# Kernel tuning notes

Hardware: AMD Instinct MI355X
Metric: run time of the kernel (lower is better)

Reference implementation:

```python
import jax, jax.numpy as jnp
import numpy as np

B, N, DIM = 2, 2048, 1024
HEADS, DIM_HEAD = 16, 64
SCALE = DIM_HEAD ** -0.5
MASK_VALUE = -jnp.finfo(jnp.float32).max


def setup_inputs() -> dict:
    key = jax.random.key(0)
    ks = jax.random.split(key, 7)
    inner = HEADS * DIM_HEAD
    x = jax.random.normal(ks[0], (B, N, DIM), dtype=jnp.float32)
    mask = jax.random.randint(ks[1], (B, 1, N, N), 0, 2, dtype=jnp.int32)
    Wq = jax.random.normal(ks[2], (DIM, inner), dtype=jnp.float32) * (DIM ** -0.5)
    Wk = jax.random.normal(ks[3], (DIM, inner), dtype=jnp.float32) * (DIM ** -0.5)
    Wv = jax.random.normal(ks[4], (DIM, inner), dtype=jnp.float32) * (DIM ** -0.5)
    Wo = jax.random.normal(ks[5], (inner, DIM), dtype=jnp.float32) * (inner ** -0.5)
    bo = jnp.zeros((DIM,), dtype=jnp.float32)
    return {"x": x, "mask": mask, "Wq": Wq, "Wk": Wk, "Wv": Wv, "Wo": Wo, "bo": bo}


def reference(x, mask, Wq, Wk, Wv, Wo, bo):
    b, n, _ = x.shape
    # projections -> [b, h, n, d]
    def split_heads(t):
        return t.reshape(b, n, HEADS, DIM_HEAD).transpose(0, 2, 1, 3)
    q = split_heads(x @ Wq)
    k = split_heads(x @ Wk)
    v = split_heads(x @ Wv)
    # full attention scores [b, h, i, j]
    dots = jnp.einsum('bhid,bhjd->bhij', q, k) * SCALE
    # faithful to source: bin_mask = (mask == 0); fill where ~bin_mask
    bin_mask = (mask == 0)
    dots = jnp.where(bin_mask, dots, MASK_VALUE)
    attn = jax.nn.softmax(dots, axis=-1)  # dropout p=0.0 -> identity
    out = jnp.einsum('bhij,bhjd->bhid', attn, v)
    out = out.transpose(0, 2, 1, 3).reshape(b, n, HEADS * DIM_HEAD)
    return out @ Wo + bo
```

## Files before the change

### kernel.cpp

```cpp
#include <hip/hip_runtime.h>
#include <cstdint>
#include <cstddef>

typedef float    f32x4  __attribute__((ext_vector_type(4)));
typedef __bf16   bf16x8 __attribute__((ext_vector_type(8)));
typedef unsigned u32x4  __attribute__((ext_vector_type(4)));
typedef unsigned u32x2  __attribute__((ext_vector_type(2)));
typedef unsigned short u16;
typedef unsigned int   u32;

#define SCL2E 0.18033688011112042f

static __device__ __forceinline__ u16 f2bf(float f) {
    u32 u = __builtin_bit_cast(u32, f);
    u32 r = (u + 0x7FFFu + ((u >> 16) & 1u)) >> 16;
    return (u16)r;
}

static __device__ __forceinline__ u32 cvtpk_bf16(float lo, float hi) {
    u32 r;
    asm("v_cvt_pk_bf16_f32 %0, %1, %2" : "=v"(r) : "v"(lo), "v"(hi));
    return r;
}

static __device__ __forceinline__ float fexp2(float x) {
    float r;
    asm("v_exp_f32 %0, %1" : "=v"(r) : "v"(x));
    return r;
}

static __device__ __forceinline__ void gll16(const u16* g, void* l) {
    __builtin_amdgcn_global_load_lds((const __attribute__((address_space(1))) void*)g,
                                     (__attribute__((address_space(3))) void*)l, 16, 0, 0);
}


__global__ __launch_bounds__(256) void prep_k(
    const float* __restrict__ x, u16* __restrict__ xb,
    const float* __restrict__ W0, const float* __restrict__ W1,
    const float* __restrict__ W2, const float* __restrict__ W3,
    u16* __restrict__ T0, u16* __restrict__ T1,
    u16* __restrict__ T2, u16* __restrict__ T3,
    const int* __restrict__ mask, u32* __restrict__ mp)
{
    __shared__ float T[64][65];
    const int bid = blockIdx.x;
    if (bid < 2048) {
        const long i = ((long)bid * 256 + threadIdx.x) * 8;
        f32x4 a = *(const f32x4*)(x + i);
        f32x4 c = *(const f32x4*)(x + i + 4);
        u32x4 o;
        o[0] = (u32)f2bf(a[0]) | ((u32)f2bf(a[1]) << 16);
        o[1] = (u32)f2bf(a[2]) | ((u32)f2bf(a[3]) << 16);
        o[2] = (u32)f2bf(c[0]) | ((u32)f2bf(c[1]) << 16);
        o[3] = (u32)f2bf(c[2]) | ((u32)f2bf(c[3]) << 16);
        *(u32x4*)(xb + i) = o;
    } else if (bid < 3072) {
        const int idx = bid - 2048;
        const int z = idx >> 8, rem = idx & 255;
        const int n0 = (rem & 15) * 64, k0 = (rem >> 4) * 64;
        const float* W = (z == 0) ? W0 : (z == 1) ? W1 : (z == 2) ? W2 : W3;
        u16* Wt = (z == 0) ? T0 : (z == 1) ? T1 : (z == 2) ? T2 : T3;
        const float scl = (z == 0) ? SCL2E : 1.0f;
        const int c = threadIdx.x & 63, r0 = (threadIdx.x >> 6) * 16;
#pragma unroll
        for (int i = 0; i < 16; ++i)
            T[r0 + i][c] = W[(long)(k0 + r0 + i) * 1024 + n0 + c];
        __syncthreads();
#pragma unroll
        for (int i = 0; i < 16; ++i)
            Wt[(long)(n0 + r0 + i) * 1024 + k0 + c] = f2bf(T[c][r0 + i] * scl);
    } else {
        const long wi = (long)(bid - 3072) * 256 + threadIdx.x;
        const int* src = mask + wi * 32;
        u32 word = 0;
#pragma unroll
        for (int c = 0; c < 8; ++c) {
            const int4 v = *(const int4*)(src + c * 4);
            word |= (u32)(v.x != 0) << (c * 4);
            word |= (u32)(v.y != 0) << (c * 4 + 1);
            word |= (u32)(v.z != 0) << (c * 4 + 2);
            word |= (u32)(v.w != 0) << (c * 4 + 3);
        }
        mp[wi] = word;
    }
}

__global__ __launch_bounds__(256) void vt_k(const u16* __restrict__ v, u16* __restrict__ vt) {
    __shared__ u16 T[64][66];
    const int nt = blockIdx.x, h = blockIdx.y, b = blockIdx.z;
    const int c = threadIdx.x & 63, r0 = (threadIdx.x >> 6) * 16;
    const u16* src = v + ((long)b * 2048 + nt * 64) * 1024 + h * 64;
    u16* dst = vt + ((long)(b * 16 + h) * 64) * 2048 + nt * 64;
#pragma unroll
    for (int i = 0; i < 16; ++i)
        T[r0 + i][c] = src[(long)(r0 + i) * 1024 + c];
    __syncthreads();
#pragma unroll
    for (int i = 0; i < 16; ++i)
        dst[(long)(r0 + i) * 2048 + c] = T[c][r0 + i];
}


__global__ __launch_bounds__(256, 3) void gemm_qkv(
    const u16* __restrict__ A, const u16* __restrict__ Bt, u16* __restrict__ C0)
{
    constexpr int K = 1024;
    __shared__ u16 As[2][128 * 32];
    __shared__ u16 Bs[2][128 * 32];
    const int tid = threadIdx.x;
    const int wave = tid >> 6, lane = tid & 63;
    const int wr = wave >> 1, wc = wave & 1;
    const int g = lane >> 4, lr = lane & 15;
    const long mBase = (long)blockIdx.y * 128;
    const long nBase = (long)blockIdx.x * 128;

    f32x4 acc[4][4];
#pragma unroll
    for (int i = 0; i < 4; ++i)
#pragma unroll
        for (int j = 0; j < 4; ++j) acc[i][j] = f32x4{0.f, 0.f, 0.f, 0.f};

    const int o0 = tid * 16, o1 = (256 + tid) * 16;
    const int r0 = o0 >> 6, cb0 = o0 & 63;
    const int r1 = o1 >> 6, cb1 = o1 & 63;

    gll16(A  + (mBase + r0) * K + (cb0 >> 1), (char*)&As[0][0] + o0);
    gll16(A  + (mBase + r1) * K + (cb1 >> 1), (char*)&As[0][0] + o1);
    gll16(Bt + (nBase + r0) * K + (cb0 >> 1), (char*)&Bs[0][0] + o0);
    gll16(Bt + (nBase + r1) * K + (cb1 >> 1), (char*)&Bs[0][0] + o1);
    __syncthreads();

#pragma unroll 2
    for (int kt = 0; kt < 32; ++kt) {
        const int buf = kt & 1;
        if (kt + 1 < 32) {
            const long ko = (long)(kt + 1) * 32;
            gll16(A  + (mBase + r0) * K + ko + (cb0 >> 1), (char*)&As[buf ^ 1][0] + o0);
            gll16(A  + (mBase + r1) * K + ko + (cb1 >> 1), (char*)&As[buf ^ 1][0] + o1);
            gll16(Bt + (nBase + r0) * K + ko + (cb0 >> 1), (char*)&Bs[buf ^ 1][0] + o0);
            gll16(Bt + (nBase + r1) * K + ko + (cb1 >> 1), (char*)&Bs[buf ^ 1][0] + o1);
        }
        bf16x8 af[4], bfv[4];
#pragma unroll
        for (int mi = 0; mi < 4; ++mi)
            af[mi] = *(const bf16x8*)((const char*)&As[buf][0] + (wr * 64 + mi * 16 + lr) * 64 + g * 16);
#pragma unroll
        for (int ni = 0; ni < 4; ++ni)
            bfv[ni] = *(const bf16x8*)((const char*)&Bs[buf][0] + (wc * 64 + ni * 16 + lr) * 64 + g * 16);
#pragma unroll
        for (int mi = 0; mi < 4; ++mi)
#pragma unroll
            for (int ni = 0; ni < 4; ++ni)
                acc[mi][ni] = __builtin_amdgcn_mfma_f32_16x16x32_bf16(af[mi], bfv[ni], acc[mi][ni], 0, 0, 0);
        __syncthreads();
    }

    const int wsel = (int)(nBase >> 10);
    u16* Cw = C0 + (long)wsel * (4096l * 1024);
    const long ncl = nBase & 1023;
#pragma unroll
    for (int mi = 0; mi < 4; ++mi)
#pragma unroll
        for (int r = 0; r < 4; ++r) {
            const long row = mBase + wr * 64 + mi * 16 + g * 4 + r;
#pragma unroll
            for (int ni = 0; ni < 4; ++ni) {
                const long col = ncl + wc * 64 + ni * 16 + lr;
                Cw[row * 1024 + col] = f2bf(acc[mi][ni][r]);
            }
        }
}


__global__ __launch_bounds__(256, 2) void gemm_out(
    const u16* __restrict__ A, const u16* __restrict__ Bt,
    float* __restrict__ Cf, const float* __restrict__ bias)
{
    constexpr int K = 1024, N = 1024;
    __shared__ u16 As[2][64 * 32];
    __shared__ u16 Bs[2][128 * 32];
    const int tid = threadIdx.x;
    const int wave = tid >> 6, lane = tid & 63;
    const int wr = wave >> 1, wc = wave & 1;
    const int g = lane >> 4, lr = lane & 15;
    const long mBase = (long)blockIdx.y * 64;
    const long nBase = (long)blockIdx.x * 128;

    f32x4 acc[2][4];
#pragma unroll
    for (int i = 0; i < 2; ++i)
#pragma unroll
        for (int j = 0; j < 4; ++j) acc[i][j] = f32x4{0.f, 0.f, 0.f, 0.f};

    const int oA = tid * 16;
    const int rA = oA >> 6, cbA = oA & 63;
    const int o0 = tid * 16, o1 = (256 + tid) * 16;
    const int r0 = o0 >> 6, cb0 = o0 & 63;
    const int r1 = o1 >> 6, cb1 = o1 & 63;

    gll16(A  + (mBase + rA) * K + (cbA >> 1), (char*)&As[0][0] + oA);
    gll16(Bt + (nBase + r0) * K + (cb0 >> 1), (char*)&Bs[0][0] + o0);
    gll16(Bt + (nBase + r1) * K + (cb1 >> 1), (char*)&Bs[0][0] + o1);
    __syncthreads();

#pragma unroll 2
    for (int kt = 0; kt < 32; ++kt) {
        const int buf = kt & 1;
        if (kt + 1 < 32) {
            const long ko = (long)(kt + 1) * 32;
            gll16(A  + (mBase + rA) * K + ko + (cbA >> 1), (char*)&As[buf ^ 1][0] + oA);
            gll16(Bt + (nBase + r0) * K + ko + (cb0 >> 1), (char*)&Bs[buf ^ 1][0] + o0);
            gll16(Bt + (nBase + r1) * K + ko + (cb1 >> 1), (char*)&Bs[buf ^ 1][0] + o1);
        }
        bf16x8 af[2], bfv[4];
#pragma unroll
        for (int mi = 0; mi < 2; ++mi)
            af[mi] = *(const bf16x8*)((const char*)&As[buf][0] + (wr * 32 + mi * 16 + lr) * 64 + g * 16);
#pragma unroll
        for (int ni = 0; ni < 4; ++ni)
            bfv[ni] = *(const bf16x8*)((const char*)&Bs[buf][0] + (wc * 64 + ni * 16 + lr) * 64 + g * 16);
#pragma unroll
        for (int mi = 0; mi < 2; ++mi)
#pragma unroll
            for (int ni = 0; ni < 4; ++ni)
                acc[mi][ni] = __builtin_amdgcn_mfma_f32_16x16x32_bf16(af[mi], bfv[ni], acc[mi][ni], 0, 0, 0);
        __syncthreads();
    }

#pragma unroll
    for (int mi = 0; mi < 2; ++mi)
#pragma unroll
        for (int r = 0; r < 4; ++r) {
            const long row = mBase + wr * 32 + mi * 16 + g * 4 + r;
#pragma unroll
            for (int ni = 0; ni < 4; ++ni) {
                const long col = nBase + wc * 64 + ni * 16 + lr;
                Cf[row * N + col] = acc[mi][ni][r] + bias[col];
            }
        }
}


__global__ __launch_bounds__(256, 2) void attn_fwd(
    const u16* __restrict__ Qg_, const u16* __restrict__ Kg_, const u16* __restrict__ Vtg_,
    const u32* __restrict__ maskp, u16* __restrict__ Og_)
{
    __shared__ u16 Ks[2][2][64 * 64];
    __shared__ u16 Vs[2][2][64 * 64];

    const int tid = threadIdx.x, w = tid >> 6, lane = tid & 63;
    const int g = lane >> 4, lr = lane & 15;
    const int L = blockIdx.x;
    const int slot = L >> 3;
    const int grp = (L & 7) + 8 * (slot >> 4);
    const int q0 = (slot & 15) * 128;
    const int b = grp >> 4, h = grp & 15;
    const u16* Qg = Qg_ + ((long)b * 2048) * 1024 + h * 64;
    const u16* Kg = Kg_ + ((long)b * 2048) * 1024 + h * 64;
    const u16* Vtg = Vtg_ + ((long)grp * 64) * 2048;
    u16* Og = Og_ + ((long)b * 2048) * 1024 + h * 64;

    long ksrc[2], vsrc[2];
    int ldso[2];
#pragma unroll
    for (int c = 0; c < 2; ++c) {
        const int o = (tid + c * 256) * 16;
        const int m = o >> 7, cb = o & 127;
        const int sb = cb ^ ((m & 7) << 4);
        ldso[c] = o;
        const int kap = ((m >> 4) & 1) * 32 + ((m >> 2) & 3) * 8 + ((m >> 5) & 1) * 4 + (m & 3);
        ksrc[c] = (long)kap * 1024 + (sb >> 1);
        vsrc[c] = (long)m * 2048 + (sb >> 1);
    }

    bf16x8 qf[2][2];
#pragma unroll
    for (int nq = 0; nq < 2; ++nq)
#pragma unroll
        for (int ks = 0; ks < 2; ++ks)
            qf[nq][ks] = *(const bf16x8*)(Qg + (long)(q0 + w * 32 + nq * 16 + lr) * 1024 + ks * 32 + g * 8);

    const long mrow0 = (long)b * 2048 + q0 + w * 32 + lr;
    const u32* mpr0 = maskp + mrow0 * 64;
    const u32* mpr1 = maskp + (mrow0 + 16) * 64;

    u32x4 mwC0 = *(const u32x4*)(mpr0);
    u32x4 mwC1 = *(const u32x4*)(mpr1);
#pragma unroll
    for (int hh = 0; hh < 2; ++hh)
#pragma unroll
        for (int c = 0; c < 2; ++c) {
            gll16(Kg + hh * 65536 + ksrc[c], (char*)&Ks[0][hh][0] + ldso[c]);
            gll16(Vtg + hh * 64 + vsrc[c], (char*)&Vs[0][hh][0] + ldso[c]);
        }
    __syncthreads();

    const int swz = (lr & 7) << 4;
    int kb[2];
#pragma unroll
    for (int ks = 0; ks < 2; ++ks) kb[ks] = (ks * 64 + g * 16) ^ swz;

    f32x4 oacc[2][4];
#pragma unroll
    for (int i = 0; i < 2; ++i)
#pragma unroll
        for (int j = 0; j < 4; ++j) oacc[i][j] = f32x4{0.f, 0.f, 0.f, 0.f};
    f32x4 osum[2];
    osum[0] = f32x4{0.f, 0.f, 0.f, 0.f};
    osum[1] = f32x4{0.f, 0.f, 0.f, 0.f};
    const f32x4 z4 = {0.f, 0.f, 0.f, 0.f};
    const u32x4 ones4 = {0x3F803F80u, 0x3F803F80u, 0x3F803F80u, 0x3F803F80u};
    const bf16x8 ones8 = __builtin_bit_cast(bf16x8, ones4);

    for (int t = 0; t < 16; ++t) {
        const int cur = t & 1;
        u32x4 mwN0, mwN1;
        if (t + 1 < 16) {
            mwN0 = *(const u32x4*)(mpr0 + (t + 1) * 4);
            mwN1 = *(const u32x4*)(mpr1 + (t + 1) * 4);
            const long kv0 = (long)(t + 1) * 128;
#pragma unroll
            for (int hh = 0; hh < 2; ++hh)
#pragma unroll
                for (int c = 0; c < 2; ++c) {
                    gll16(Kg + (kv0 + hh * 64) * 1024 + ksrc[c], (char*)&Ks[cur ^ 1][hh][0] + ldso[c]);
                    gll16(Vtg + kv0 + hh * 64 + vsrc[c], (char*)&Vs[cur ^ 1][hh][0] + ldso[c]);
                }
        }

#pragma unroll
        for (int hh = 0; hh < 2; ++hh) {
            const char* kbase = (const char*)&Ks[cur][hh][0];
            const char* vbase = (const char*)&Vs[cur][hh][0];

            f32x4 s[4][2];
            __builtin_amdgcn_s_setprio(1);
#pragma unroll
            for (int mt = 0; mt < 4; ++mt) {
                const bf16x8 kf0 = *(const bf16x8*)(kbase + (mt * 16 + lr) * 128 + kb[0]);
                const bf16x8 kf1 = *(const bf16x8*)(kbase + (mt * 16 + lr) * 128 + kb[1]);
#pragma unroll
                for (int nq = 0; nq < 2; ++nq) {
                    s[mt][nq] = __builtin_amdgcn_mfma_f32_16x16x32_bf16(kf0, qf[nq][0], z4, 0, 0, 0);
                    s[mt][nq] = __builtin_amdgcn_mfma_f32_16x16x32_bf16(kf1, qf[nq][1], s[mt][nq], 0, 0, 0);
                }
            }
            __builtin_amdgcn_s_setprio(0);

            u32 pk[4][2][2];
#pragma unroll
            for (int ts = 0; ts < 4; ++ts) {
                const int sh = g * 8 + (ts >> 1) * 4;
                const int wi = hh * 2 + (ts & 1);
#pragma unroll
                for (int nq = 0; nq < 2; ++nq) {
                    const u32 word = nq ? mwC1[wi] : mwC0[wi];
                    const u32 wsh = word >> sh;
                    float e[4];
#pragma unroll
                    for (int r = 0; r < 4; ++r) {
                        const float sv = ((wsh >> r) & 1u) ? -512.f : s[ts][nq][r];
                        e[r] = fexp2(sv);
                    }
                    pk[ts][nq][0] = cvtpk_bf16(e[0], e[1]);
                    pk[ts][nq][1] = cvtpk_bf16(e[2], e[3]);
                }
            }

            bf16x8 pa[2][2];
#pragma unroll
            for (int nq = 0; nq < 2; ++nq)
#pragma unroll
                for (int ks = 0; ks < 2; ++ks) {
                    u32x4 t4;
                    t4[0] = pk[ks][nq][0]; t4[1] = pk[ks][nq][1];
                    t4[2] = pk[ks + 2][nq][0]; t4[3] = pk[ks + 2][nq][1];
                    pa[nq][ks] = __builtin_bit_cast(bf16x8, t4);
                }
            __builtin_amdgcn_s_setprio(1);
#pragma unroll
            for (int nq = 0; nq < 2; ++nq)
#pragma unroll
                for (int ks = 0; ks < 2; ++ks)
                    osum[nq] = __builtin_amdgcn_mfma_f32_16x16x32_bf16(pa[nq][ks], ones8, osum[nq], 0, 0, 0);
#pragma unroll
            for (int dt = 0; dt < 4; ++dt)
#pragma unroll
                for (int ks = 0; ks < 2; ++ks) {
                    const bf16x8 vf = *(const bf16x8*)(vbase + (dt * 16 + lr) * 128 + kb[ks]);
#pragma unroll
                    for (int nq = 0; nq < 2; ++nq)
                        oacc[nq][dt] = __builtin_amdgcn_mfma_f32_16x16x32_bf16(pa[nq][ks], vf, oacc[nq][dt], 0, 0, 0);
                }
            __builtin_amdgcn_s_setprio(0);
        }
        __syncthreads();

        mwC0 = mwN0; mwC1 = mwN1;
    }

#pragma unroll
    for (int nq = 0; nq < 2; ++nq)
#pragma unroll
        for (int rr = 0; rr < 4; ++rr) {
            const float inv = __builtin_amdgcn_rcpf(osum[nq][rr]);
            const long row = (long)q0 + w * 32 + nq * 16 + g * 4 + rr;
#pragma unroll
            for (int dt = 0; dt < 4; ++dt)
                Og[row * 1024 + dt * 16 + lr] = f2bf(oacc[nq][dt][rr] * inv);
        }
}


extern "C" void kernel_launch(void* const* d_in, const int* in_sizes, int n_in,
                              void* d_out, int out_size, void* d_ws, size_t ws_size,
                              hipStream_t stream)
{
    (void)in_sizes; (void)n_in; (void)out_size; (void)ws_size;
    const float* x    = (const float*)d_in[0];
    const int*   mask = (const int*)d_in[1];
    const float* Wq   = (const float*)d_in[2];
    const float* Wk   = (const float*)d_in[3];
    const float* Wv   = (const float*)d_in[4];
    const float* Wo   = (const float*)d_in[5];
    const float* bo   = (const float*)d_in[6];
    float* out = (float*)d_out;

    char* ws = (char*)d_ws;
    u16* xb    = (u16*)(ws);
    u16* vtws  = (u16*)(ws);
    u16* WqT   = (u16*)(ws + (8l  << 20));
    u16* WkT   = (u16*)(ws + (10l << 20));
    u16* WvT   = (u16*)(ws + (12l << 20));
    u16* WoT   = (u16*)(ws + (14l << 20));
    u16* qws   = (u16*)(ws + (16l << 20));
    u16* kws   = (u16*)(ws + (24l << 20));
    u16* vws   = (u16*)(ws + (32l << 20));
    u16* inner = (u16*)(ws + (40l << 20));
    u32* mp    = (u32*)(ws + (48l << 20));

    prep_k<<<4096, 256, 0, stream>>>(x, xb, Wq, Wk, Wv, Wo, WqT, WkT, WvT, WoT, mask, mp);
    gemm_qkv<<<dim3(24, 32), 256, 0, stream>>>(xb, WqT, qws);
    vt_k<<<dim3(32, 16, 2), 256, 0, stream>>>(vws, vtws);
    attn_fwd<<<512, 256, 0, stream>>>(qws, kws, vtws, mp, inner);
    gemm_out<<<dim3(8, 64), 256, 0, stream>>>(inner, WoT, out, bo);
}
```

Before: 135.5 us.

## Double attention block to 512 threads and 256 queries sharing each K/V tile

```diff
diff --git a/kernel.cpp b/kernel.cpp
--- a/kernel.cpp
+++ b/kernel.cpp
@@ -242,7 +242,7 @@
 }
 
 
-__global__ __launch_bounds__(256, 2) void attn_fwd(
+__global__ __launch_bounds__(512, 2) void attn_fwd(
     const u16* __restrict__ Qg_, const u16* __restrict__ Kg_, const u16* __restrict__ Vtg_,
     const u32* __restrict__ maskp, u16* __restrict__ Og_)
 {
@@ -253,26 +253,20 @@
     const int g = lane >> 4, lr = lane & 15;
     const int L = blockIdx.x;
     const int slot = L >> 3;
-    const int grp = (L & 7) + 8 * (slot >> 4);
-    const int q0 = (slot & 15) * 128;
+    const int grp = (L & 7) + 8 * (slot >> 3);
+    const int q0 = (slot & 7) * 256;
     const int b = grp >> 4, h = grp & 15;
     const u16* Qg = Qg_ + ((long)b * 2048) * 1024 + h * 64;
     const u16* Kg = Kg_ + ((long)b * 2048) * 1024 + h * 64;
     const u16* Vtg = Vtg_ + ((long)grp * 64) * 2048;
     u16* Og = Og_ + ((long)b * 2048) * 1024 + h * 64;
 
-    long ksrc[2], vsrc[2];
-    int ldso[2];
-#pragma unroll
-    for (int c = 0; c < 2; ++c) {
-        const int o = (tid + c * 256) * 16;
-        const int m = o >> 7, cb = o & 127;
-        const int sb = cb ^ ((m & 7) << 4);
-        ldso[c] = o;
-        const int kap = ((m >> 4) & 1) * 32 + ((m >> 2) & 3) * 8 + ((m >> 5) & 1) * 4 + (m & 3);
-        ksrc[c] = (long)kap * 1024 + (sb >> 1);
-        vsrc[c] = (long)m * 2048 + (sb >> 1);
-    }
+    const int ldso = tid * 16;
+    const int m = ldso >> 7, cb = ldso & 127;
+    const int sb = cb ^ ((m & 7) << 4);
+    const int kap = ((m >> 4) & 1) * 32 + ((m >> 2) & 3) * 8 + ((m >> 5) & 1) * 4 + (m & 3);
+    const long ksrc = (long)kap * 1024 + (sb >> 1);
+    const long vsrc = (long)m * 2048 + (sb >> 1);
 
     bf16x8 qf[2][2];
 #pragma unroll
@@ -288,12 +282,10 @@
     u32x4 mwC0 = *(const u32x4*)(mpr0);
     u32x4 mwC1 = *(const u32x4*)(mpr1);
 #pragma unroll
-    for (int hh = 0; hh < 2; ++hh)
-#pragma unroll
-        for (int c = 0; c < 2; ++c) {
-            gll16(Kg + hh * 65536 + ksrc[c], (char*)&Ks[0][hh][0] + ldso[c]);
-            gll16(Vtg + hh * 64 + vsrc[c], (char*)&Vs[0][hh][0] + ldso[c]);
-        }
+    for (int hh = 0; hh < 2; ++hh) {
+        gll16(Kg + hh * 65536 + ksrc, (char*)&Ks[0][hh][0] + ldso);
+        gll16(Vtg + hh * 64 + vsrc, (char*)&Vs[0][hh][0] + ldso);
+    }
     __syncthreads();
 
     const int swz = (lr & 7) << 4;
@@ -313,6 +305,7 @@
     const u32x4 ones4 = {0x3F803F80u, 0x3F803F80u, 0x3F803F80u, 0x3F803F80u};
     const bf16x8 ones8 = __builtin_bit_cast(bf16x8, ones4);
 
+#pragma unroll 2
     for (int t = 0; t < 16; ++t) {
         const int cur = t & 1;
         u32x4 mwN0, mwN1;
@@ -321,12 +314,10 @@
             mwN1 = *(const u32x4*)(mpr1 + (t + 1) * 4);
             const long kv0 = (long)(t + 1) * 128;
 #pragma unroll
-            for (int hh = 0; hh < 2; ++hh)
-#pragma unroll
-                for (int c = 0; c < 2; ++c) {
-                    gll16(Kg + (kv0 + hh * 64) * 1024 + ksrc[c], (char*)&Ks[cur ^ 1][hh][0] + ldso[c]);
-                    gll16(Vtg + kv0 + hh * 64 + vsrc[c], (char*)&Vs[cur ^ 1][hh][0] + ldso[c]);
-                }
+            for (int hh = 0; hh < 2; ++hh) {
+                gll16(Kg + (kv0 + hh * 64) * 1024 + ksrc, (char*)&Ks[cur ^ 1][hh][0] + ldso);
+                gll16(Vtg + kv0 + hh * 64 + vsrc, (char*)&Vs[cur ^ 1][hh][0] + ldso);
+            }
         }
 
 #pragma unroll
@@ -356,12 +347,13 @@
 #pragma unroll
                 for (int nq = 0; nq < 2; ++nq) {
                     const u32 word = nq ? mwC1[wi] : mwC0[wi];
-                    const u32 wsh = word >> sh;
+                    const u32 iwsh = (~word) >> sh;
                     float e[4];
 #pragma unroll
                     for (int r = 0; r < 4; ++r) {
-                        const float sv = ((wsh >> r) & 1u) ? -512.f : s[ts][nq][r];
-                        e[r] = fexp2(sv);
+                        const float ev = fexp2(s[ts][nq][r]);
+                        const u32 keep = (u32)__builtin_amdgcn_sbfe((int)iwsh, (u32)r, 1u);
+                        e[r] = __builtin_bit_cast(float, __builtin_bit_cast(u32, ev) & keep);
                     }
                     pk[ts][nq][0] = cvtpk_bf16(e[0], e[1]);
                     pk[ts][nq][1] = cvtpk_bf16(e[2], e[3]);
@@ -443,6 +435,6 @@
     prep_k<<<4096, 256, 0, stream>>>(x, xb, Wq, Wk, Wv, Wo, WqT, WkT, WvT, WoT, mask, mp);
     gemm_qkv<<<dim3(24, 32), 256, 0, stream>>>(xb, WqT, qws);
     vt_k<<<dim3(32, 16, 2), 256, 0, stream>>>(vws, vtws);
-    attn_fwd<<<512, 256, 0, stream>>>(qws, kws, vtws, mp, inner);
+    attn_fwd<<<256, 512, 0, stream>>>(qws, kws, vtws, mp, inner);
     gemm_out<<<dim3(8, 64), 256, 0, stream>>>(inner, WoT, out, bo);
 }
```

After: 130.6 us. 1.04x faster.
